# Kernel optimization log

Measured on AMD Instinct MI355X. Metric: run time of the kernel, lower is better.

Reference implementation:

```python
import jax, jax.numpy as jnp
import numpy as np

DIM = 320
NUM_HEADS = 5
HEAD_DIM = DIM // NUM_HEADS  # 64
SCALE = HEAD_DIM ** -0.5


def setup_inputs() -> dict:
    key = jax.random.key(0)
    k1, k2, k3, k4 = jax.random.split(key, 4)
    B, N, C = 8, 2048, DIM
    x = jax.random.normal(k1, (B, N, C), dtype=jnp.float32)
    # nn.Linear(dim, dim*3, bias=False): weight [3*dim, dim]
    w_qkv = jax.random.normal(k2, (3 * C, C), dtype=jnp.float32) * (C ** -0.5)
    # nn.Linear(dim, dim): weight [dim, dim], bias [dim]
    w_proj = jax.random.normal(k3, (C, C), dtype=jnp.float32) * (C ** -0.5)
    b_proj = jax.random.normal(k4, (C,), dtype=jnp.float32) * 0.01
    return {"x": x, "w_qkv": w_qkv, "w_proj": w_proj, "b_proj": b_proj}


def reference(x, w_qkv, w_proj, b_proj):
    B, N, C = x.shape
    H, D = NUM_HEADS, HEAD_DIM
    # qkv projection: [B, N, 3C] -> [3, B, H, N, D]
    qkv = jnp.einsum('bnc,kc->bnk', x, w_qkv)
    qkv = qkv.reshape(B, N, 3, H, D).transpose(2, 0, 3, 1, 4)
    q, k, v = qkv[0], qkv[1], qkv[2]
    # full attention matrix [B, H, N, N] (retained by original module)
    attn = jnp.einsum('bhnd,bhmd->bhnm', q, k) * SCALE
    attn = jax.nn.softmax(attn, axis=-1)
    # attn_drop p=0 -> identity (eval/deterministic)
    out = jnp.einsum('bhnm,bhmd->bhnd', attn, v)
    out = out.transpose(0, 2, 1, 3).reshape(B, N, C)
    out = jnp.einsum('bnc,oc->bno', out, w_proj) + b_proj
    # proj_drop p=0 -> identity
    return out
```

## Files before the change

### kernel.cpp

```cpp
#include <hip/hip_runtime.h>
#include <hip/hip_bf16.h>


typedef __attribute__((ext_vector_type(8))) short bf16x8;
typedef __attribute__((ext_vector_type(4))) float f32x4;

#define MFMA(a, b, c) __builtin_amdgcn_mfma_f32_16x16x32_bf16((a), (b), (c), 0, 0, 0)

#define QSCALE 0.18033688322643216f

static __device__ inline bf16x8 ld8(const __hip_bfloat16* p) {
    return *reinterpret_cast<const bf16x8*>(p);
}

static __device__ inline unsigned short bfbits(float v) {
    unsigned int u = __builtin_bit_cast(unsigned int, v);
    u += 0x7FFFu + ((u >> 16) & 1u);
    return (unsigned short)(u >> 16);
}

static __device__ inline unsigned int cvtpk(float lo, float hi) {
    unsigned int r;
    asm("v_cvt_pk_bf16_f32 %0, %1, %2" : "=v"(r) : "v"(lo), "v"(hi));
    return r;
}

static __device__ inline bf16x8 cvt8(const float* src) {
    float4 a = *reinterpret_cast<const float4*>(src);
    float4 b = *reinterpret_cast<const float4*>(src + 4);
    bf16x8 v;
    v[0] = (short)bfbits(a.x); v[1] = (short)bfbits(a.y);
    v[2] = (short)bfbits(a.z); v[3] = (short)bfbits(a.w);
    v[4] = (short)bfbits(b.x); v[5] = (short)bfbits(b.y);
    v[6] = (short)bfbits(b.z); v[7] = (short)bfbits(b.w);
    return v;
}

__global__ __launch_bounds__(256)
void cvt_x(const float* __restrict__ x, __hip_bfloat16* __restrict__ xb)
{
    const size_t tid = (size_t)blockIdx.x * blockDim.x + threadIdx.x;
    const size_t stride = (size_t)gridDim.x * blockDim.x;
    const float4* x4 = (const float4*)x;
    ushort4* xb4 = (ushort4*)xb;
    for (size_t i = tid; i < 1310720u; i += stride) {
        float4 v = x4[i];
        ushort4 u;
        u.x = bfbits(v.x); u.y = bfbits(v.y);
        u.z = bfbits(v.z); u.w = bfbits(v.w);
        xb4[i] = u;
    }
}

__global__ __launch_bounds__(256)
void qkv_kernel(const __hip_bfloat16* __restrict__ xb,
                const float* __restrict__ w,
                __hip_bfloat16* __restrict__ qout,
                __hip_bfloat16* __restrict__ kp,
                __hip_bfloat16* __restrict__ vp)
{
    __shared__ __align__(16) __hip_bfloat16 As[128 * 72];
    __shared__ __align__(16) __hip_bfloat16 Bs[64 * 72];

    const int tid  = threadIdx.x;
    const int wv   = tid >> 6;
    const int lane = tid & 63;
    const int quad = lane >> 4;
    const int col  = lane & 15;
    const int m0   = blockIdx.x * 128;
    const int n0   = blockIdx.y * 64;

    f32x4 acc[2][4];
#pragma unroll
    for (int i = 0; i < 2; ++i)
#pragma unroll
        for (int j = 0; j < 4; ++j) acc[i][j] = (f32x4){0.f, 0.f, 0.f, 0.f};

    for (int k0 = 0; k0 < 320; k0 += 64) {
        __syncthreads();
#pragma unroll
        for (int i = 0; i < 4; ++i) {
            int ch = tid + i * 256;
            int r = ch >> 3, sg = ch & 7;
            *reinterpret_cast<float4*>(&As[r * 72 + sg * 8]) =
                *reinterpret_cast<const float4*>(&xb[(m0 + r) * 320 + k0 + sg * 8]);
        }
#pragma unroll
        for (int i = 0; i < 2; ++i) {
            int ch = tid + i * 256;
            int r = ch >> 3, sg = ch & 7;
            *reinterpret_cast<bf16x8*>(&Bs[r * 72 + sg * 8]) =
                cvt8(&w[(n0 + r) * 320 + k0 + sg * 8]);
        }
        __syncthreads();

#pragma unroll
        for (int hf = 0; hf < 2; ++hf) {
            bf16x8 a0 = ld8(&As[(wv * 32 + col) * 72 + hf * 32 + quad * 8]);
            bf16x8 a1 = ld8(&As[(wv * 32 + 16 + col) * 72 + hf * 32 + quad * 8]);
#pragma unroll
            for (int nt = 0; nt < 4; ++nt) {
                bf16x8 b = ld8(&Bs[(nt * 16 + col) * 72 + hf * 32 + quad * 8]);
                acc[0][nt] = MFMA(a0, b, acc[0][nt]);
                acc[1][nt] = MFMA(a1, b, acc[1][nt]);
            }
        }
    }

    const int s = blockIdx.y / 5;
    const int h = blockIdx.y % 5;
    unsigned short* qo = (unsigned short*)qout;
    unsigned short* ko = (unsigned short*)kp;
    unsigned short* vo = (unsigned short*)vp;
#pragma unroll
    for (int mt = 0; mt < 2; ++mt) {
#pragma unroll
        for (int nt = 0; nt < 4; ++nt) {
#pragma unroll
            for (int r = 0; r < 4; ++r) {
                int m = m0 + wv * 32 + mt * 16 + quad * 4 + r;
                int d = nt * 16 + col;
                int b = m >> 11, n = m & 2047;
                int bh = b * 5 + h;
                float val = acc[mt][nt][r];
                if (s == 0) {
                    qo[((size_t)bh * 2048 + n) * 64 + d] = bfbits(val * QSCALE);
                } else if (s == 1) {
                    int p = n >> 6, nn = n & 63;
                    size_t a = ((size_t)(bh * 32 + p) * 8 + (d >> 5) * 4 + (nn >> 4)) * 512
                             + (((d >> 3) & 3) * 16 + (nn & 15)) * 8 + (d & 7);
                    ko[a] = bfbits(val);
                } else {
                    int p = n >> 6;
                    size_t a = ((size_t)(bh * 32 + p) * 8 + ((n >> 5) & 1) * 4 + (d >> 4)) * 512
                             + (((n >> 3) & 3) * 16 + (d & 15)) * 8 + (n & 7);
                    vo[a] = bfbits(val);
                }
            }
        }
    }
}

__global__ __launch_bounds__(128)
void attn_kernel(const __hip_bfloat16* __restrict__ Q,
                 const __hip_bfloat16* __restrict__ Kp,
                 const __hip_bfloat16* __restrict__ Vp,
                 __hip_bfloat16* __restrict__ A2)
{
    __shared__ __align__(16) unsigned char smraw[9216];

    const int tid  = threadIdx.x;
    const int wv   = tid >> 6;
    const int lane = tid & 63;
    const int quad = lane >> 4;
    const int col  = lane & 15;
    const int bh = blockIdx.y, b = bh / 5, h = bh % 5;
    const int q0 = blockIdx.x * 32;
    const int t0 = wv * 16;

    char* psb = (char*)smraw + wv * 4608;
    char* ps_w = psb + col * 144 + quad * 8;
    const __hip_bfloat16* ps_r =
        (const __hip_bfloat16*)psb + col * 72 + quad * 8;

    const __hip_bfloat16* kt = Kp + (size_t)bh * 131072 + (size_t)t0 * 4096 + lane * 8;
    const __hip_bfloat16* vt = Vp + (size_t)bh * 131072 + (size_t)t0 * 4096 + lane * 8;
    const __hip_bfloat16* Qh = Q + (size_t)bh * 131072;

    bf16x8 qf[2][2];
#pragma unroll
    for (int mt = 0; mt < 2; ++mt)
#pragma unroll
        for (int hf = 0; hf < 2; ++hf)
            qf[mt][hf] = ld8(&Qh[(q0 + mt * 16 + col) * 64 + hf * 32 + quad * 8]);

    f32x4 lp[2];
    f32x4 o[2][4];
#pragma unroll
    for (int mt = 0; mt < 2; ++mt) {
        lp[mt] = (f32x4){0.f, 0.f, 0.f, 0.f};
#pragma unroll
        for (int dt = 0; dt < 4; ++dt) o[mt][dt] = (f32x4){0.f, 0.f, 0.f, 0.f};
    }

    bf16x8 ka[8];
#pragma unroll
    for (int f = 0; f < 8; ++f) ka[f] = ld8(kt + f * 512);
    kt += 4096;

    for (int t = 0; t < 16; ++t) {
        f32x4 s[2][4];
#pragma unroll
        for (int mt = 0; mt < 2; ++mt)
#pragma unroll
            for (int nt = 0; nt < 4; ++nt) {
                f32x4 z = (f32x4){0.f, 0.f, 0.f, 0.f};
                z = MFMA(ka[nt], qf[mt][0], z);
                z = MFMA(ka[4 + nt], qf[mt][1], z);
                s[mt][nt] = z;
            }

        bf16x8 va[8];
#pragma unroll
        for (int f = 0; f < 8; ++f) va[f] = ld8(vt + f * 512);
        vt += 4096;

#pragma unroll
        for (int f = 0; f < 8; ++f) ka[f] = ld8(kt + f * 512);
        kt += 4096;

#pragma unroll
        for (int mt = 0; mt < 2; ++mt)
#pragma unroll
            for (int nt = 0; nt < 4; ++nt) {
                f32x4 pv;
#pragma unroll
                for (int r = 0; r < 4; ++r)
                    pv[r] = __builtin_amdgcn_exp2f(s[mt][nt][r]);
                lp[mt] += pv;
                uint2 wpk;
                wpk.x = cvtpk(pv[0], pv[1]);
                wpk.y = cvtpk(pv[2], pv[3]);
                *reinterpret_cast<uint2*>(ps_w + mt * 2304 + nt * 32) = wpk;
            }
        __asm__ volatile("s_waitcnt lgkmcnt(0)" ::: "memory");

#pragma unroll
        for (int mt = 0; mt < 2; ++mt)
#pragma unroll
            for (int kk = 0; kk < 2; ++kk) {
                bf16x8 pf = ld8(ps_r + mt * 1152 + kk * 32);
#pragma unroll
                for (int dt = 0; dt < 4; ++dt)
                    o[mt][dt] = MFMA(pf, va[kk * 4 + dt], o[mt][dt]);
            }
    }

    float lsum[2];
#pragma unroll
    for (int mt = 0; mt < 2; ++mt) {
        float v = lp[mt][0] + lp[mt][1] + lp[mt][2] + lp[mt][3];
        v += __shfl_xor(v, 16, 64);
        v += __shfl_xor(v, 32, 64);
        lsum[mt] = v;
    }

    float* cbo = (float*)smraw;
    float* lw  = cbo + 2048;
    __syncthreads();
    if (wv == 1) {
#pragma unroll
        for (int mt = 0; mt < 2; ++mt)
#pragma unroll
            for (int dt = 0; dt < 4; ++dt)
#pragma unroll
                for (int r = 0; r < 4; ++r)
                    cbo[(mt * 16 + quad * 4 + r) * 64 + dt * 16 + col] = o[mt][dt][r];
    }
    if (quad == 0) {
#pragma unroll
        for (int mt = 0; mt < 2; ++mt)
            lw[wv * 32 + mt * 16 + col] = lsum[mt];
    }
    __syncthreads();
    if (wv == 0) {
        unsigned short* a2o = (unsigned short*)A2;
#pragma unroll
        for (int mt = 0; mt < 2; ++mt) {
#pragma unroll
            for (int r = 0; r < 4; ++r) {
                int row = mt * 16 + quad * 4 + r;
                float inv = 1.0f / (lw[row] + lw[32 + row]);
                int grow = q0 + row;
#pragma unroll
                for (int dt = 0; dt < 4; ++dt) {
                    int d = dt * 16 + col;
                    float val = (o[mt][dt][r] + cbo[row * 64 + d]) * inv;
                    a2o[((size_t)(b * 2048 + grow)) * 320 + h * 64 + d] = bfbits(val);
                }
            }
        }
    }
}

__global__ __launch_bounds__(256)
void proj_kernel(const __hip_bfloat16* __restrict__ a2,
                 const float* __restrict__ w,
                 const float* __restrict__ bias,
                 float* __restrict__ out)
{
    __shared__ __align__(16) __hip_bfloat16 As[128 * 72];
    __shared__ __align__(16) __hip_bfloat16 Bs[64 * 72];

    const int tid  = threadIdx.x;
    const int wv   = tid >> 6;
    const int lane = tid & 63;
    const int quad = lane >> 4;
    const int col  = lane & 15;
    const int m0   = blockIdx.x * 128;
    const int n0   = blockIdx.y * 64;

    f32x4 acc[2][4];
#pragma unroll
    for (int i = 0; i < 2; ++i)
#pragma unroll
        for (int j = 0; j < 4; ++j) acc[i][j] = (f32x4){0.f, 0.f, 0.f, 0.f};

    for (int k0 = 0; k0 < 320; k0 += 64) {
        __syncthreads();
#pragma unroll
        for (int i = 0; i < 4; ++i) {
            int ch = tid + i * 256;
            int r = ch >> 3, sg = ch & 7;
            *reinterpret_cast<float4*>(&As[r * 72 + sg * 8]) =
                *reinterpret_cast<const float4*>(&a2[(m0 + r) * 320 + k0 + sg * 8]);
        }
#pragma unroll
        for (int i = 0; i < 2; ++i) {
            int ch = tid + i * 256;
            int r = ch >> 3, sg = ch & 7;
            *reinterpret_cast<bf16x8*>(&Bs[r * 72 + sg * 8]) =
                cvt8(&w[(n0 + r) * 320 + k0 + sg * 8]);
        }
        __syncthreads();

#pragma unroll
        for (int hf = 0; hf < 2; ++hf) {
            bf16x8 a0 = ld8(&As[(wv * 32 + col) * 72 + hf * 32 + quad * 8]);
            bf16x8 a1 = ld8(&As[(wv * 32 + 16 + col) * 72 + hf * 32 + quad * 8]);
#pragma unroll
            for (int nt = 0; nt < 4; ++nt) {
                bf16x8 b = ld8(&Bs[(nt * 16 + col) * 72 + hf * 32 + quad * 8]);
                acc[0][nt] = MFMA(a0, b, acc[0][nt]);
                acc[1][nt] = MFMA(a1, b, acc[1][nt]);
            }
        }
    }

#pragma unroll
    for (int nt = 0; nt < 4; ++nt) {
        float bv = bias[n0 + nt * 16 + col];
#pragma unroll
        for (int mt = 0; mt < 2; ++mt) {
#pragma unroll
            for (int r = 0; r < 4; ++r) {
                int m = m0 + wv * 32 + mt * 16 + quad * 4 + r;
                out[(size_t)m * 320 + n0 + nt * 16 + col] = acc[mt][nt][r] + bv;
            }
        }
    }
}

extern "C" void kernel_launch(void* const* d_in, const int* in_sizes, int n_in,
                              void* d_out, int out_size, void* d_ws, size_t ws_size,
                              hipStream_t stream)
{
    const float* x      = (const float*)d_in[0];
    const float* w_qkv  = (const float*)d_in[1];
    const float* w_proj = (const float*)d_in[2];
    const float* b_proj = (const float*)d_in[3];
    float* out = (float*)d_out;

    const size_t NX = 5242880;
    __hip_bfloat16* xb = (__hip_bfloat16*)d_ws;
    __hip_bfloat16* q  = xb + NX;
    __hip_bfloat16* kp = q + NX;
    __hip_bfloat16* vp = kp + NX;
    __hip_bfloat16* a2 = xb;

    cvt_x<<<1024, 256, 0, stream>>>(x, xb);
    qkv_kernel<<<dim3(128, 15), 256, 0, stream>>>(xb, w_qkv, q, kp, vp);
    attn_kernel<<<dim3(64, 40), 128, 0, stream>>>(q, kp, vp, a2);
    proj_kernel<<<dim3(128, 5), 256, 0, stream>>>(a2, w_proj, b_proj, out);
}
```

Measured before the change: 180.6 us.

## Share K/V tiles via LDS double-buffering across four query-splitting waves

The attention kernel goes from 2 waves that split the key range to 4 waves that each own 32 query rows over the full key range. K/V tiles are copied into double-buffered shared memory with direct global-to-LDS loads, so all four waves reuse one copy. Blocks are remapped so each XCD works on a fixed set of heads, which should improve L2 locality. The cross-wave output reduction is gone, but every key tile now costs a block barrier, and K/V fragments are read from LDS instead of registers.

After: 171.9 us. 4.8% less time.

```diff
diff --git a/kernel.cpp b/kernel.cpp
--- a/kernel.cpp
+++ b/kernel.cpp
@@ -23,6 +23,12 @@
     unsigned int r;
     asm("v_cvt_pk_bf16_f32 %0, %1, %2" : "=v"(r) : "v"(lo), "v"(hi));
     return r;
+}
+
+static __device__ inline void gload_lds16(const __hip_bfloat16* g, __hip_bfloat16* l) {
+    __builtin_amdgcn_global_load_lds(
+        (const __attribute__((address_space(1))) void*)g,
+        (__attribute__((address_space(3))) void*)l, 16, 0, 0);
 }
 
 static __device__ inline bf16x8 cvt8(const float* src) {
@@ -141,30 +147,35 @@
     }
 }
 
-__global__ __launch_bounds__(128)
+__global__ __launch_bounds__(256)
 void attn_kernel(const __hip_bfloat16* __restrict__ Q,
                  const __hip_bfloat16* __restrict__ Kp,
                  const __hip_bfloat16* __restrict__ Vp,
                  __hip_bfloat16* __restrict__ A2)
 {
-    __shared__ __align__(16) unsigned char smraw[9216];
+    __shared__ __align__(16) __hip_bfloat16 KV[16384];
+    __shared__ __align__(16) unsigned char psraw[18432];
 
     const int tid  = threadIdx.x;
     const int wv   = tid >> 6;
     const int lane = tid & 63;
     const int quad = lane >> 4;
     const int col  = lane & 15;
-    const int bh = blockIdx.y, b = bh / 5, h = bh % 5;
-    const int q0 = blockIdx.x * 32;
-    const int t0 = wv * 16;
-
-    char* psb = (char*)smraw + wv * 4608;
+
+    const int id  = blockIdx.x;
+    const int xcd = id & 7;
+    const int j   = id >> 3;
+    const int bh  = xcd * 5 + (j >> 4);
+    const int q0w = (j & 15) * 128 + wv * 32;
+    const int b   = bh / 5, h = bh % 5;
+
+    char* psb = (char*)psraw + wv * 4608;
     char* ps_w = psb + col * 144 + quad * 8;
     const __hip_bfloat16* ps_r =
         (const __hip_bfloat16*)psb + col * 72 + quad * 8;
 
-    const __hip_bfloat16* kt = Kp + (size_t)bh * 131072 + (size_t)t0 * 4096 + lane * 8;
-    const __hip_bfloat16* vt = Vp + (size_t)bh * 131072 + (size_t)t0 * 4096 + lane * 8;
+    const __hip_bfloat16* kg = Kp + (size_t)bh * 131072;
+    const __hip_bfloat16* vg = Vp + (size_t)bh * 131072;
     const __hip_bfloat16* Qh = Q + (size_t)bh * 131072;
 
     bf16x8 qf[2][2];
@@ -172,7 +183,7 @@
     for (int mt = 0; mt < 2; ++mt)
 #pragma unroll
         for (int hf = 0; hf < 2; ++hf)
-            qf[mt][hf] = ld8(&Qh[(q0 + mt * 16 + col) * 64 + hf * 32 + quad * 8]);
+            qf[mt][hf] = ld8(&Qh[(q0w + mt * 16 + col) * 64 + hf * 32 + quad * 8]);
 
     f32x4 lp[2];
     f32x4 o[2][4];
@@ -183,31 +194,41 @@
         for (int dt = 0; dt < 4; ++dt) o[mt][dt] = (f32x4){0.f, 0.f, 0.f, 0.f};
     }
 
-    bf16x8 ka[8];
-#pragma unroll
-    for (int f = 0; f < 8; ++f) ka[f] = ld8(kt + f * 512);
-    kt += 4096;
-
-    for (int t = 0; t < 16; ++t) {
+    auto stage = [&](int t, int c) {
+        const __hip_bfloat16* kp_ = kg + (size_t)t * 4096 + wv * 1024 + lane * 8;
+        const __hip_bfloat16* vp_ = vg + (size_t)t * 4096 + wv * 1024 + lane * 8;
+        __hip_bfloat16* kl = &KV[c * 4096 + wv * 1024];
+        __hip_bfloat16* vl = &KV[8192 + c * 4096 + wv * 1024];
+        gload_lds16(kp_, kl);
+        gload_lds16(kp_ + 512, kl + 512);
+        gload_lds16(vp_, vl);
+        gload_lds16(vp_ + 512, vl + 512);
+    };
+
+    stage(0, 0);
+
+    for (int t = 0; t < 32; ++t) {
+        const int c = t & 1;
+        asm volatile("s_waitcnt vmcnt(0)" ::: "memory");
+        __builtin_amdgcn_s_barrier();
+        stage((t < 31) ? t + 1 : 31, c ^ 1);
+
+        const __hip_bfloat16* kb = &KV[c * 4096];
+        const __hip_bfloat16* vb = &KV[8192 + c * 4096];
+
         f32x4 s[2][4];
 #pragma unroll
-        for (int mt = 0; mt < 2; ++mt)
-#pragma unroll
-            for (int nt = 0; nt < 4; ++nt) {
+        for (int nt = 0; nt < 4; ++nt) {
+            bf16x8 k0 = ld8(kb + nt * 512 + lane * 8);
+            bf16x8 k1 = ld8(kb + (4 + nt) * 512 + lane * 8);
+#pragma unroll
+            for (int mt = 0; mt < 2; ++mt) {
                 f32x4 z = (f32x4){0.f, 0.f, 0.f, 0.f};
-                z = MFMA(ka[nt], qf[mt][0], z);
-                z = MFMA(ka[4 + nt], qf[mt][1], z);
+                z = MFMA(k0, qf[mt][0], z);
+                z = MFMA(k1, qf[mt][1], z);
                 s[mt][nt] = z;
             }
-
-        bf16x8 va[8];
-#pragma unroll
-        for (int f = 0; f < 8; ++f) va[f] = ld8(vt + f * 512);
-        vt += 4096;
-
-#pragma unroll
-        for (int f = 0; f < 8; ++f) ka[f] = ld8(kt + f * 512);
-        kt += 4096;
+        }
 
 #pragma unroll
         for (int mt = 0; mt < 2; ++mt)
@@ -231,8 +252,10 @@
             for (int kk = 0; kk < 2; ++kk) {
                 bf16x8 pf = ld8(ps_r + mt * 1152 + kk * 32);
 #pragma unroll
-                for (int dt = 0; dt < 4; ++dt)
-                    o[mt][dt] = MFMA(pf, va[kk * 4 + dt], o[mt][dt]);
+                for (int dt = 0; dt < 4; ++dt) {
+                    bf16x8 va = ld8(vb + (kk * 4 + dt) * 512 + lane * 8);
+                    o[mt][dt] = MFMA(pf, va, o[mt][dt]);
+                }
             }
     }
 
@@ -245,39 +268,27 @@
         lsum[mt] = v;
     }
 
-    float* cbo = (float*)smraw;
-    float* lw  = cbo + 2048;
-    __syncthreads();
-    if (wv == 1) {
+    float* lw = (float*)psb;
+    if (quad == 0) {
 #pragma unroll
         for (int mt = 0; mt < 2; ++mt)
-#pragma unroll
-            for (int dt = 0; dt < 4; ++dt)
-#pragma unroll
-                for (int r = 0; r < 4; ++r)
-                    cbo[(mt * 16 + quad * 4 + r) * 64 + dt * 16 + col] = o[mt][dt][r];
-    }
-    if (quad == 0) {
-#pragma unroll
-        for (int mt = 0; mt < 2; ++mt)
-            lw[wv * 32 + mt * 16 + col] = lsum[mt];
-    }
-    __syncthreads();
-    if (wv == 0) {
-        unsigned short* a2o = (unsigned short*)A2;
-#pragma unroll
-        for (int mt = 0; mt < 2; ++mt) {
-#pragma unroll
-            for (int r = 0; r < 4; ++r) {
-                int row = mt * 16 + quad * 4 + r;
-                float inv = 1.0f / (lw[row] + lw[32 + row]);
-                int grow = q0 + row;
-#pragma unroll
-                for (int dt = 0; dt < 4; ++dt) {
-                    int d = dt * 16 + col;
-                    float val = (o[mt][dt][r] + cbo[row * 64 + d]) * inv;
-                    a2o[((size_t)(b * 2048 + grow)) * 320 + h * 64 + d] = bfbits(val);
-                }
+            lw[mt * 16 + col] = lsum[mt];
+    }
+    __asm__ volatile("s_waitcnt lgkmcnt(0)" ::: "memory");
+
+    unsigned short* a2o = (unsigned short*)A2;
+#pragma unroll
+    for (int mt = 0; mt < 2; ++mt) {
+#pragma unroll
+        for (int r = 0; r < 4; ++r) {
+            int row = mt * 16 + quad * 4 + r;
+            float inv = 1.0f / lw[row];
+            int grow = q0w + row;
+#pragma unroll
+            for (int dt = 0; dt < 4; ++dt) {
+                int d = dt * 16 + col;
+                a2o[((size_t)(b * 2048 + grow)) * 320 + h * 64 + d] =
+                    bfbits(o[mt][dt][r] * inv);
             }
         }
     }
@@ -370,6 +381,6 @@
 
     cvt_x<<<1024, 256, 0, stream>>>(x, xb);
     qkv_kernel<<<dim3(128, 15), 256, 0, stream>>>(xb, w_qkv, q, kp, vp);
-    attn_kernel<<<dim3(64, 40), 128, 0, stream>>>(q, kp, vp, a2);
+    attn_kernel<<<640, 256, 0, stream>>>(q, kp, vp, a2);
     proj_kernel<<<dim3(128, 5), 256, 0, stream>>>(a2, w_proj, b_proj, out);
 }
```
